# Optimization experiments

Measured on AMD Instinct MI355X. Metric: run time of the kernel, lower is better.

The kernel has to match this reference:

```python
import jax, jax.numpy as jnp
import numpy as np

N = 50000      # nodes
E = 800000     # edges (avg degree 16)
IN_DIM, HID, OUT = 128, 128, 64
EPS = 1e-5     # BatchNorm1d eps


def setup_inputs() -> dict:
    key = jax.random.key(0)
    ks = jax.random.split(key, 8)
    x = jax.random.normal(ks[0], (N, IN_DIM), jnp.float32)
    edge_index = jax.random.randint(ks[1], (2, E), 0, N, dtype=jnp.int32)
    def lin(k, i, o):
        return jax.random.normal(k, (i, o), jnp.float32) / np.sqrt(i).astype(np.float32)
    return {
        "x": x,
        "edge_index": edge_index,
        "W1": lin(ks[2], IN_DIM, HID), "b1": jnp.zeros((HID,), jnp.float32),
        "g1": jnp.ones((HID,), jnp.float32), "beta1": jnp.zeros((HID,), jnp.float32),
        "W2": lin(ks[3], HID, HID), "b2": jnp.zeros((HID,), jnp.float32),
        "g2": jnp.ones((HID,), jnp.float32), "beta2": jnp.zeros((HID,), jnp.float32),
        "W3": lin(ks[4], HID, OUT), "b3": jnp.zeros((OUT,), jnp.float32),
    }


def reference(x, edge_index, W1, b1, g1, beta1, W2, b2, g2, beta2, W3, b3):
    # GCNConv normalization: add self-loops, sym norm D^-1/2 (A+I) D^-1/2
    loops = jnp.arange(N, dtype=edge_index.dtype)
    src = jnp.concatenate([edge_index[0], loops])  # message sources
    dst = jnp.concatenate([edge_index[1], loops])  # aggregation targets
    deg = jax.ops.segment_sum(jnp.ones_like(dst, jnp.float32), dst, num_segments=N)
    dis = jnp.where(deg > 0, jax.lax.rsqrt(jnp.maximum(deg, 1.0)), 0.0)
    norm = dis[src] * dis[dst]  # [E+N]

    def conv(h, W, b):
        h = h @ W  # lin before propagation (PyG GCNConv)
        agg = jax.ops.segment_sum(h[src] * norm[:, None], dst, num_segments=N)
        return agg + b  # bias after aggregation

    def bn(h, g, beta):
        # training-mode BatchNorm1d: batch stats over node dim (biased var)
        m = h.mean(axis=0)
        v = h.var(axis=0)
        return g * (h - m) * jax.lax.rsqrt(v + EPS) + beta

    h = jax.nn.relu(bn(conv(x, W1, b1), g1, beta1))   # dropout deterministic (identity)
    h = jax.nn.relu(bn(conv(h, W2, b2), g2, beta2))
    h = conv(h, W3, b3)
    return jax.nn.log_softmax(h, axis=-1)
```

## Files before the change

### kernel.cpp

```cpp
#include <hip/hip_runtime.h>
#include <hip/hip_fp16.h>
#include <math.h>

#define N_NODES 50000
#define N_EDGES 800000
#define BN_EPS 1e-5f
#define CAP 64
#define NPART 256
#define PART 196
#define CHUNK_CAP 48

typedef _Float16 f16x8 __attribute__((ext_vector_type(8)));
typedef float f32x4 __attribute__((ext_vector_type(4)));

constexpr int GB = (N_NODES + 63) / 64;
constexpr int AB = (N_NODES + 3) / 4;
constexpr int EPB = N_EDGES / NPART;

__global__ __launch_bounds__(256) void setup_partA_k(
    const int* __restrict__ ei, unsigned int* __restrict__ chunk, int* __restrict__ cntT,
    const float* __restrict__ W1, const float* __restrict__ W2, const float* __restrict__ W3,
    __half* __restrict__ Wt1, __half* __restrict__ Wt2, __half* __restrict__ Wt3,
    int* __restrict__ fil, float* __restrict__ sums) {
    if (blockIdx.x < NPART) {
        __shared__ int cnt[NPART];
        int tid = threadIdx.x, b = blockIdx.x;
        cnt[tid] = 0;
        __syncthreads();
        int lo = b * EPB, hi = lo + EPB;
        for (int e = lo + tid; e < hi; e += 256) {
            int src = ei[e], dst = ei[N_EDGES + e];
            int p = dst / PART;
            int pos = atomicAdd(&cnt[p], 1);
            if (pos < CHUNK_CAP)
                chunk[(unsigned)((b << 8) + p) * CHUNK_CAP + pos] =
                    ((unsigned)dst << 16) | (unsigned)src;
        }
        __syncthreads();
        cntT[tid * NPART + b] = min(cnt[tid], CHUNK_CAP);
    } else {
        int i = (blockIdx.x - NPART) * 256 + threadIdx.x;
        if (i < N_NODES) fil[i] = 0;
        if (i < 512) sums[i] = 0.f;
        if (i < 16384) {
            int k = i >> 7, m = i & 127;
            Wt1[m * 128 + k] = __float2half(W1[i]);
            Wt2[m * 128 + k] = __float2half(W2[i]);
        }
        if (i < 8192) {
            int k = i >> 6, m = i & 63;
            Wt3[m * 128 + k] = __float2half(W3[i]);
        }
    }
}

template <int M, int AF32, int FUSE, int DSCALE>
__device__ __forceinline__ void gemm_body(int bid, int tid,
                                          const void* __restrict__ Av,
                                          const __half* __restrict__ Wt,
                                          const float* __restrict__ scale,
                                          const float* __restrict__ shift,
                                          const int* __restrict__ fil,
                                          __half* __restrict__ out) {
    constexpr int NF = M / 32;
    int wid = tid >> 6, lane = tid & 63;

    int rbase = bid * 64 + (wid >> 1) * 32;
    int ncol0 = (wid & 1) * (M / 2);
    int koff = (lane >> 4) * 8;

    int arow[2];
#pragma unroll
    for (int mi = 0; mi < 2; ++mi) {
        int r = rbase + mi * 16 + (lane & 15);
        arow[mi] = (r < N_NODES) ? r : (N_NODES - 1);
    }

    f32x4 acc[2][NF];
#pragma unroll
    for (int mi = 0; mi < 2; ++mi)
#pragma unroll
        for (int ni = 0; ni < NF; ++ni) acc[mi][ni] = (f32x4)(0.f);

#pragma unroll
    for (int k0 = 0; k0 < 128; k0 += 32) {
        float scv[8], shv[8];
        if constexpr (FUSE) {
            *(float4*)scv = *(const float4*)(scale + k0 + koff);
            *(float4*)(scv + 4) = *(const float4*)(scale + k0 + koff + 4);
            *(float4*)shv = *(const float4*)(shift + k0 + koff);
            *(float4*)(shv + 4) = *(const float4*)(shift + k0 + koff + 4);
        }
        f16x8 a[2], b[NF];
#pragma unroll
        for (int mi = 0; mi < 2; ++mi) {
            if constexpr (AF32) {
                const float* Af = (const float*)Av + (size_t)arow[mi] * 128 + k0 + koff;
                float4 p0 = *(const float4*)Af;
                float4 p1 = *(const float4*)(Af + 4);
                a[mi][0] = (_Float16)p0.x; a[mi][1] = (_Float16)p0.y;
                a[mi][2] = (_Float16)p0.z; a[mi][3] = (_Float16)p0.w;
                a[mi][4] = (_Float16)p1.x; a[mi][5] = (_Float16)p1.y;
                a[mi][6] = (_Float16)p1.z; a[mi][7] = (_Float16)p1.w;
            } else {
                f16x8 raw = *(const f16x8*)((const __half*)Av + (size_t)arow[mi] * 128 + k0 + koff);
                if constexpr (FUSE) {
#pragma unroll
                    for (int j = 0; j < 8; ++j)
                        a[mi][j] = (_Float16)fmaxf((float)raw[j] * scv[j] + shv[j], 0.f);
                } else {
                    a[mi] = raw;
                }
            }
        }
#pragma unroll
        for (int ni = 0; ni < NF; ++ni)
            b[ni] = *(const f16x8*)(Wt + (size_t)(ncol0 + ni * 16 + (lane & 15)) * 128 + k0 + koff);
#pragma unroll
        for (int mi = 0; mi < 2; ++mi)
#pragma unroll
            for (int ni = 0; ni < NF; ++ni)
                acc[mi][ni] = __builtin_amdgcn_mfma_f32_16x16x32_f16(a[mi], b[ni], acc[mi][ni], 0, 0, 0);
    }

    int ccol = ncol0 + (lane & 15);
#pragma unroll
    for (int mi = 0; mi < 2; ++mi)
#pragma unroll
        for (int q = 0; q < 4; ++q) {
            int grow = rbase + mi * 16 + (lane >> 4) * 4 + q;
            if (grow < N_NODES) {
                float ds = DSCALE ? rsqrtf((float)fil[grow] + 1.f) : 1.0f;
#pragma unroll
                for (int ni = 0; ni < NF; ++ni)
                    out[(size_t)grow * M + ccol + ni * 16] = __float2half(acc[mi][ni][q] * ds);
            }
        }
}

template <int M, int AF32, int FUSE, int DSCALE>
__global__ __launch_bounds__(256) void mfma_gemm_k(const void* __restrict__ Av,
                                                   const __half* __restrict__ Wt,
                                                   const float* __restrict__ scale,
                                                   const float* __restrict__ shift,
                                                   const int* __restrict__ fil,
                                                   __half* __restrict__ out) {
    gemm_body<M, AF32, FUSE, DSCALE>(blockIdx.x, threadIdx.x, Av, Wt, scale, shift, fil, out);
}

__global__ __launch_bounds__(256) void partB_gemm1_k(const float* __restrict__ x,
                                                     const __half* __restrict__ Wt1,
                                                     __half* __restrict__ outh,
                                                     const unsigned int* __restrict__ chunk,
                                                     const int* __restrict__ cntT,
                                                     int* __restrict__ fil,
                                                     unsigned short* __restrict__ bkt) {
    if (blockIdx.x < NPART) {
        int p = blockIdx.x, t = threadIdx.x;
        int n = cntT[p * NPART + t];
        const unsigned int* cp = chunk + (unsigned)((t << 8) + p) * CHUNK_CAP;
        for (int i = 0; i < n; ++i) {
            unsigned int u = cp[i];
            int dst = u >> 16, src = u & 0xffff;
            int pos = atomicAdd(&fil[dst], 1);
            if (pos < CAP) bkt[dst * CAP + pos] = (unsigned short)src;
        }
    } else {
        gemm_body<128, 1, 0, 0>(blockIdx.x - NPART, threadIdx.x, x, Wt1, nullptr, nullptr,
                                nullptr, outh);
    }
}

template <int SRCDIS>
__global__ __launch_bounds__(256) void aggh_k(const __half* __restrict__ hs,
                                              const int* __restrict__ fil,
                                              const unsigned short* __restrict__ bkt,
                                              const float* __restrict__ bias,
                                              __half* __restrict__ out) {
    int dst = blockIdx.x * 4 + (threadIdx.x >> 6);
    if (dst >= N_NODES) return;
    int lane = threadIdx.x & 63;
    int cnt = fil[dst];
    int n = min(cnt, CAP);
    float dd = rsqrtf((float)cnt + 1.f);
    const __half2* h2 = (const __half2*)hs;
    float2 v = __half22float2(h2[(size_t)dst * 64 + lane]);
    float ax, ay;
    if constexpr (SRCDIS) { ax = dd * v.x; ay = dd * v.y; }
    else { ax = v.x; ay = v.y; }
    const unsigned short* bp = bkt + (size_t)dst * CAP;
    int e = 0;
    for (; e + 4 <= n; e += 4) {
        int s0 = bp[e], s1 = bp[e + 1], s2 = bp[e + 2], s3 = bp[e + 3];
        float2 v0 = __half22float2(h2[(size_t)s0 * 64 + lane]);
        float2 v1 = __half22float2(h2[(size_t)s1 * 64 + lane]);
        float2 v2 = __half22float2(h2[(size_t)s2 * 64 + lane]);
        float2 v3 = __half22float2(h2[(size_t)s3 * 64 + lane]);
        if constexpr (SRCDIS) {
            float w0 = rsqrtf((float)fil[s0] + 1.f);
            float w1 = rsqrtf((float)fil[s1] + 1.f);
            float w2 = rsqrtf((float)fil[s2] + 1.f);
            float w3 = rsqrtf((float)fil[s3] + 1.f);
            ax += w0 * v0.x + w1 * v1.x + w2 * v2.x + w3 * v3.x;
            ay += w0 * v0.y + w1 * v1.y + w2 * v2.y + w3 * v3.y;
        } else {
            ax += (v0.x + v1.x) + (v2.x + v3.x);
            ay += (v0.y + v1.y) + (v2.y + v3.y);
        }
    }
    for (; e < n; ++e) {
        int s = bp[e];
        float2 vv = __half22float2(h2[(size_t)s * 64 + lane]);
        float w = SRCDIS ? rsqrtf((float)fil[s] + 1.f) : 1.0f;
        ax += w * vv.x;
        ay += w * vv.y;
    }
    float2 b = *(const float2*)(bias + lane * 2);
    ((__half2*)out)[(size_t)dst * 64 + lane] =
        __float22half2_rn(make_float2(dd * ax + b.x, dd * ay + b.y));
}

__global__ __launch_bounds__(256) void stats_k(const __half* __restrict__ h,
                                               float* __restrict__ sum, float* __restrict__ sq) {
    __shared__ float ssum[128], ssq[128];
    int tid = threadIdx.x;
    if (tid < 128) { ssum[tid] = 0.f; ssq[tid] = 0.f; }
    __syncthreads();
    float s[8], q[8];
#pragma unroll
    for (int j = 0; j < 8; ++j) { s[j] = 0.f; q[j] = 0.f; }
    const int total = N_NODES * 16;
    int stride = gridDim.x * blockDim.x;
    for (int i = blockIdx.x * blockDim.x + tid; i < total; i += stride) {
        f16x8 v = ((const f16x8*)h)[i];
#pragma unroll
        for (int j = 0; j < 8; ++j) {
            float f = (float)v[j];
            s[j] += f;
            q[j] += f * f;
        }
    }
#pragma unroll
    for (int j = 0; j < 8; ++j) {
        s[j] += __shfl_xor(s[j], 16); s[j] += __shfl_xor(s[j], 32);
        q[j] += __shfl_xor(q[j], 16); q[j] += __shfl_xor(q[j], 32);
    }
    int lane = tid & 63;
    if (lane < 16) {
        int c0 = lane * 8;
#pragma unroll
        for (int j = 0; j < 8; ++j) {
            atomicAdd(&ssum[c0 + j], s[j]);
            atomicAdd(&ssq[c0 + j], q[j]);
        }
    }
    __syncthreads();
    if (tid < 128) {
        atomicAdd(&sum[tid], ssum[tid]);
        atomicAdd(&sq[tid], ssq[tid]);
    }
}

__global__ void finalize_k(const float* __restrict__ sum, const float* __restrict__ sq,
                           const float* __restrict__ g, const float* __restrict__ beta,
                           float* scale, float* shift) {
    int f = threadIdx.x;
    float m = sum[f] * (1.0f / N_NODES);
    float v = sq[f] * (1.0f / N_NODES) - m * m;
    float sc = g[f] * rsqrtf(v + BN_EPS);
    scale[f] = sc;
    shift[f] = beta[f] - m * sc;
}

__global__ __launch_bounds__(256) void agg64sm_k(const __half* __restrict__ hs,
                                                 const int* __restrict__ fil,
                                                 const unsigned short* __restrict__ bkt,
                                                 const float* __restrict__ bias,
                                                 float* __restrict__ out) {
    int dst = blockIdx.x * 4 + (threadIdx.x >> 6);
    if (dst >= N_NODES) return;
    int lane = threadIdx.x & 63;
    int cnt = fil[dst];
    int n = min(cnt, CAP);
    float dd = rsqrtf((float)cnt + 1.f);
    float acc = __half2float(hs[(size_t)dst * 64 + lane]);
    const unsigned short* bp = bkt + (size_t)dst * CAP;
    int e = 0;
    for (; e + 4 <= n; e += 4) {
        int s0 = bp[e], s1 = bp[e + 1], s2 = bp[e + 2], s3 = bp[e + 3];
        float v0 = __half2float(hs[(size_t)s0 * 64 + lane]);
        float v1 = __half2float(hs[(size_t)s1 * 64 + lane]);
        float v2 = __half2float(hs[(size_t)s2 * 64 + lane]);
        float v3 = __half2float(hs[(size_t)s3 * 64 + lane]);
        acc += (v0 + v1) + (v2 + v3);
    }
    for (; e < n; ++e) acc += __half2float(hs[(size_t)bp[e] * 64 + lane]);
    float v = dd * acc + bias[lane];
    float m = v;
#pragma unroll
    for (int off = 32; off; off >>= 1) m = fmaxf(m, __shfl_xor(m, off));
    float p = expf(v - m);
    float ssum = p;
#pragma unroll
    for (int off = 32; off; off >>= 1) ssum += __shfl_xor(ssum, off);
    out[(size_t)dst * 64 + lane] = v - m - logf(ssum);
}

extern "C" void kernel_launch(void* const* d_in, const int* in_sizes, int n_in,
                              void* d_out, int out_size, void* d_ws, size_t ws_size,
                              hipStream_t stream) {
    const float* x = (const float*)d_in[0];
    const int* ei = (const int*)d_in[1];
    const float* W1 = (const float*)d_in[2];
    const float* b1 = (const float*)d_in[3];
    const float* g1 = (const float*)d_in[4];
    const float* be1 = (const float*)d_in[5];
    const float* W2 = (const float*)d_in[6];
    const float* b2 = (const float*)d_in[7];
    const float* g2 = (const float*)d_in[8];
    const float* be2 = (const float*)d_in[9];
    const float* W3 = (const float*)d_in[10];
    const float* b3 = (const float*)d_in[11];
    float* out = (float*)d_out;

    char* p = (char*)d_ws;
    auto alloc = [&](size_t bytes) {
        void* r = (void*)p;
        p += (bytes + 255) & ~(size_t)255;
        return r;
    };
    int* fil = (int*)alloc(N_NODES * 4);
    unsigned short* bkt = (unsigned short*)alloc((size_t)N_NODES * CAP * 2);
    unsigned int* chunk = (unsigned int*)alloc((size_t)NPART * NPART * CHUNK_CAP * 4);
    int* cntT = (int*)alloc(NPART * NPART * 4);
    float* sums = (float*)alloc(512 * 4);
    float* ss = (float*)alloc(512 * 4);
    __half* Wt1 = (__half*)alloc(128 * 128 * 2);
    __half* Wt2 = (__half*)alloc(128 * 128 * 2);
    __half* Wt3 = (__half*)alloc(64 * 128 * 2);
    __half* bufP = (__half*)alloc((size_t)N_NODES * 128 * 2);
    __half* bufQ = (__half*)alloc((size_t)N_NODES * 128 * 2);

    setup_partA_k<<<NPART + 196, 256, 0, stream>>>(ei, chunk, cntT, W1, W2, W3, Wt1, Wt2,
                                                   Wt3, fil, sums);

    partB_gemm1_k<<<NPART + GB, 256, 0, stream>>>(x, Wt1, bufQ, chunk, cntT, fil, bkt);
    aggh_k<1><<<AB, 256, 0, stream>>>(bufQ, fil, bkt, b1, bufP);
    stats_k<<<1024, 256, 0, stream>>>(bufP, sums, sums + 128);
    finalize_k<<<1, 128, 0, stream>>>(sums, sums + 128, g1, be1, ss, ss + 128);

    mfma_gemm_k<128, 0, 1, 1><<<GB, 256, 0, stream>>>(bufP, Wt2, ss, ss + 128, fil, bufQ);
    aggh_k<0><<<AB, 256, 0, stream>>>(bufQ, fil, bkt, b2, bufP);
    stats_k<<<1024, 256, 0, stream>>>(bufP, sums + 256, sums + 384);
    finalize_k<<<1, 128, 0, stream>>>(sums + 256, sums + 384, g2, be2, ss + 256, ss + 384);

    mfma_gemm_k<64, 0, 1, 1><<<GB, 256, 0, stream>>>(bufP, Wt3, ss + 256, ss + 384, fil, bufQ);
    agg64sm_k<<<AB, 256, 0, stream>>>(bufQ, fil, bkt, b3, out);
}
```

Baseline: 257.3 us.

## Vectorize gather aggregation with quarter-wave per neighbor and vectorized GEMM stores

The aggregation kernels now split each wave into four 16-lane groups, each gathering a different neighbor row with wide 16-byte (or 8-byte) loads, then combine the partial sums with cross-lane shuffles. The goal is fewer, wider memory transactions and more gathers in flight per wave than the old one-element-per-lane scheme. The GEMM swaps the MFMA operands so each lane holds four consecutive columns, which allows packed f16x4 stores instead of scalar half stores. The costs are extra shuffle reductions, idle lanes in the remainder handling, and only one quarter of the wave doing the final write.

```diff
diff --git a/kernel.cpp b/kernel.cpp
--- a/kernel.cpp
+++ b/kernel.cpp
@@ -11,6 +11,7 @@
 #define CHUNK_CAP 48
 
 typedef _Float16 f16x8 __attribute__((ext_vector_type(8)));
+typedef _Float16 f16x4 __attribute__((ext_vector_type(4)));
 typedef float f32x4 __attribute__((ext_vector_type(4)));
 
 constexpr int GB = (N_NODES + 63) / 64;
@@ -120,22 +121,24 @@
         for (int mi = 0; mi < 2; ++mi)
 #pragma unroll
             for (int ni = 0; ni < NF; ++ni)
-                acc[mi][ni] = __builtin_amdgcn_mfma_f32_16x16x32_f16(a[mi], b[ni], acc[mi][ni], 0, 0, 0);
-    }
-
-    int ccol = ncol0 + (lane & 15);
-#pragma unroll
-    for (int mi = 0; mi < 2; ++mi)
-#pragma unroll
-        for (int q = 0; q < 4; ++q) {
-            int grow = rbase + mi * 16 + (lane >> 4) * 4 + q;
-            if (grow < N_NODES) {
-                float ds = DSCALE ? rsqrtf((float)fil[grow] + 1.f) : 1.0f;
-#pragma unroll
-                for (int ni = 0; ni < NF; ++ni)
-                    out[(size_t)grow * M + ccol + ni * 16] = __float2half(acc[mi][ni][q] * ds);
+                acc[mi][ni] = __builtin_amdgcn_mfma_f32_16x16x32_f16(b[ni], a[mi], acc[mi][ni], 0, 0, 0);
+    }
+
+    int cg = lane >> 4;
+#pragma unroll
+    for (int mi = 0; mi < 2; ++mi) {
+        int grow = rbase + mi * 16 + (lane & 15);
+        if (grow < N_NODES) {
+            float ds = DSCALE ? rsqrtf((float)fil[grow] + 1.f) : 1.0f;
+#pragma unroll
+            for (int ni = 0; ni < NF; ++ni) {
+                f16x4 hv;
+#pragma unroll
+                for (int q = 0; q < 4; ++q) hv[q] = (_Float16)(acc[mi][ni][q] * ds);
+                *(f16x4*)(out + (size_t)grow * M + ncol0 + ni * 16 + cg * 4) = hv;
             }
         }
+    }
 }
 
 template <int M, int AF32, int FUSE, int DSCALE>
@@ -180,44 +183,74 @@
     int dst = blockIdx.x * 4 + (threadIdx.x >> 6);
     if (dst >= N_NODES) return;
     int lane = threadIdx.x & 63;
+    int qw = lane >> 4, li = lane & 15;
     int cnt = fil[dst];
     int n = min(cnt, CAP);
     float dd = rsqrtf((float)cnt + 1.f);
-    const __half2* h2 = (const __half2*)hs;
-    float2 v = __half22float2(h2[(size_t)dst * 64 + lane]);
-    float ax, ay;
-    if constexpr (SRCDIS) { ax = dd * v.x; ay = dd * v.y; }
-    else { ax = v.x; ay = v.y; }
+    const f16x8* h8 = (const f16x8*)hs;
+
+    float acc[8];
+    {
+        f16x8 sv = h8[(size_t)dst * 16 + li];
+        float selfw = (qw == 0) ? (SRCDIS ? dd : 1.f) : 0.f;
+#pragma unroll
+        for (int j = 0; j < 8; ++j) acc[j] = selfw * (float)sv[j];
+    }
+
     const unsigned short* bp = bkt + (size_t)dst * CAP;
     int e = 0;
+    for (; e + 8 <= n; e += 8) {
+        ushort4 ua = *(const ushort4*)(bp + e);
+        ushort4 ub = *(const ushort4*)(bp + e + 4);
+        int sa = (qw == 0) ? ua.x : (qw == 1) ? ua.y : (qw == 2) ? ua.z : ua.w;
+        int sb = (qw == 0) ? ub.x : (qw == 1) ? ub.y : (qw == 2) ? ub.z : ub.w;
+        f16x8 va = h8[(size_t)sa * 16 + li];
+        f16x8 vb = h8[(size_t)sb * 16 + li];
+        float wa = 1.f, wb = 1.f;
+        if constexpr (SRCDIS) {
+            wa = rsqrtf((float)fil[sa] + 1.f);
+            wb = rsqrtf((float)fil[sb] + 1.f);
+        }
+#pragma unroll
+        for (int j = 0; j < 8; ++j) acc[j] += wa * (float)va[j] + wb * (float)vb[j];
+    }
     for (; e + 4 <= n; e += 4) {
-        int s0 = bp[e], s1 = bp[e + 1], s2 = bp[e + 2], s3 = bp[e + 3];
-        float2 v0 = __half22float2(h2[(size_t)s0 * 64 + lane]);
-        float2 v1 = __half22float2(h2[(size_t)s1 * 64 + lane]);
-        float2 v2 = __half22float2(h2[(size_t)s2 * 64 + lane]);
-        float2 v3 = __half22float2(h2[(size_t)s3 * 64 + lane]);
-        if constexpr (SRCDIS) {
-            float w0 = rsqrtf((float)fil[s0] + 1.f);
-            float w1 = rsqrtf((float)fil[s1] + 1.f);
-            float w2 = rsqrtf((float)fil[s2] + 1.f);
-            float w3 = rsqrtf((float)fil[s3] + 1.f);
-            ax += w0 * v0.x + w1 * v1.x + w2 * v2.x + w3 * v3.x;
-            ay += w0 * v0.y + w1 * v1.y + w2 * v2.y + w3 * v3.y;
-        } else {
-            ax += (v0.x + v1.x) + (v2.x + v3.x);
-            ay += (v0.y + v1.y) + (v2.y + v3.y);
-        }
-    }
-    for (; e < n; ++e) {
-        int s = bp[e];
-        float2 vv = __half22float2(h2[(size_t)s * 64 + lane]);
-        float w = SRCDIS ? rsqrtf((float)fil[s] + 1.f) : 1.0f;
-        ax += w * vv.x;
-        ay += w * vv.y;
-    }
-    float2 b = *(const float2*)(bias + lane * 2);
-    ((__half2*)out)[(size_t)dst * 64 + lane] =
-        __float22half2_rn(make_float2(dd * ax + b.x, dd * ay + b.y));
+        ushort4 u = *(const ushort4*)(bp + e);
+        int s = (qw == 0) ? u.x : (qw == 1) ? u.y : (qw == 2) ? u.z : u.w;
+        f16x8 v = h8[(size_t)s * 16 + li];
+        float w = 1.f;
+        if constexpr (SRCDIS) w = rsqrtf((float)fil[s] + 1.f);
+#pragma unroll
+        for (int j = 0; j < 8; ++j) acc[j] += w * (float)v[j];
+    }
+    if (e < n) {
+        int rem = n - e;
+        ushort4 u = *(const ushort4*)(bp + e);
+        int s = (qw == 0) ? u.x : (qw == 1) ? u.y : (qw == 2) ? u.z : u.w;
+        if (qw < rem) {
+            f16x8 v = h8[(size_t)s * 16 + li];
+            float w = 1.f;
+            if constexpr (SRCDIS) w = rsqrtf((float)fil[s] + 1.f);
+#pragma unroll
+            for (int j = 0; j < 8; ++j) acc[j] += w * (float)v[j];
+        }
+    }
+
+#pragma unroll
+    for (int j = 0; j < 8; ++j) {
+        acc[j] += __shfl_xor(acc[j], 16);
+        acc[j] += __shfl_xor(acc[j], 32);
+    }
+
+    if (qw == 0) {
+        float bv[8];
+        *(float4*)bv = *(const float4*)(bias + li * 8);
+        *(float4*)(bv + 4) = *(const float4*)(bias + li * 8 + 4);
+        f16x8 o;
+#pragma unroll
+        for (int j = 0; j < 8; ++j) o[j] = (_Float16)(dd * acc[j] + bv[j]);
+        *(f16x8*)(out + (size_t)dst * 128 + li * 8) = o;
+    }
 }
 
 __global__ __launch_bounds__(256) void stats_k(const __half* __restrict__ h,
@@ -280,30 +313,74 @@
     int dst = blockIdx.x * 4 + (threadIdx.x >> 6);
     if (dst >= N_NODES) return;
     int lane = threadIdx.x & 63;
+    int qw = lane >> 4, li = lane & 15;
     int cnt = fil[dst];
     int n = min(cnt, CAP);
     float dd = rsqrtf((float)cnt + 1.f);
-    float acc = __half2float(hs[(size_t)dst * 64 + lane]);
+    const f16x4* h4 = (const f16x4*)hs;
+
+    float acc[4];
+    {
+        f16x4 sv = h4[(size_t)dst * 16 + li];
+        float selfw = (qw == 0) ? 1.f : 0.f;
+#pragma unroll
+        for (int j = 0; j < 4; ++j) acc[j] = selfw * (float)sv[j];
+    }
+
     const unsigned short* bp = bkt + (size_t)dst * CAP;
     int e = 0;
+    for (; e + 8 <= n; e += 8) {
+        ushort4 ua = *(const ushort4*)(bp + e);
+        ushort4 ub = *(const ushort4*)(bp + e + 4);
+        int sa = (qw == 0) ? ua.x : (qw == 1) ? ua.y : (qw == 2) ? ua.z : ua.w;
+        int sb = (qw == 0) ? ub.x : (qw == 1) ? ub.y : (qw == 2) ? ub.z : ub.w;
+        f16x4 va = h4[(size_t)sa * 16 + li];
+        f16x4 vb = h4[(size_t)sb * 16 + li];
+#pragma unroll
+        for (int j = 0; j < 4; ++j) acc[j] += (float)va[j] + (float)vb[j];
+    }
     for (; e + 4 <= n; e += 4) {
-        int s0 = bp[e], s1 = bp[e + 1], s2 = bp[e + 2], s3 = bp[e + 3];
-        float v0 = __half2float(hs[(size_t)s0 * 64 + lane]);
-        float v1 = __half2float(hs[(size_t)s1 * 64 + lane]);
-        float v2 = __half2float(hs[(size_t)s2 * 64 + lane]);
-        float v3 = __half2float(hs[(size_t)s3 * 64 + lane]);
-        acc += (v0 + v1) + (v2 + v3);
-    }
-    for (; e < n; ++e) acc += __half2float(hs[(size_t)bp[e] * 64 + lane]);
-    float v = dd * acc + bias[lane];
-    float m = v;
-#pragma unroll
-    for (int off = 32; off; off >>= 1) m = fmaxf(m, __shfl_xor(m, off));
-    float p = expf(v - m);
-    float ssum = p;
-#pragma unroll
-    for (int off = 32; off; off >>= 1) ssum += __shfl_xor(ssum, off);
-    out[(size_t)dst * 64 + lane] = v - m - logf(ssum);
+        ushort4 u = *(const ushort4*)(bp + e);
+        int s = (qw == 0) ? u.x : (qw == 1) ? u.y : (qw == 2) ? u.z : u.w;
+        f16x4 v = h4[(size_t)s * 16 + li];
+#pragma unroll
+        for (int j = 0; j < 4; ++j) acc[j] += (float)v[j];
+    }
+    if (e < n) {
+        int rem = n - e;
+        ushort4 u = *(const ushort4*)(bp + e);
+        int s = (qw == 0) ? u.x : (qw == 1) ? u.y : (qw == 2) ? u.z : u.w;
+        if (qw < rem) {
+            f16x4 v = h4[(size_t)s * 16 + li];
+#pragma unroll
+            for (int j = 0; j < 4; ++j) acc[j] += (float)v[j];
+        }
+    }
+
+#pragma unroll
+    for (int j = 0; j < 4; ++j) {
+        acc[j] += __shfl_xor(acc[j], 16);
+        acc[j] += __shfl_xor(acc[j], 32);
+    }
+
+    float bv[4];
+    *(float4*)bv = *(const float4*)(bias + li * 4);
+    float v[4];
+#pragma unroll
+    for (int j = 0; j < 4; ++j) v[j] = dd * acc[j] + bv[j];
+
+    float m = fmaxf(fmaxf(v[0], v[1]), fmaxf(v[2], v[3]));
+#pragma unroll
+    for (int off = 8; off; off >>= 1) m = fmaxf(m, __shfl_xor(m, off));
+    float p = expf(v[0] - m) + expf(v[1] - m) + expf(v[2] - m) + expf(v[3] - m);
+#pragma unroll
+    for (int off = 8; off; off >>= 1) p += __shfl_xor(p, off);
+    float lse = m + logf(p);
+
+    if (qw == 0) {
+        float4 o = make_float4(v[0] - lse, v[1] - lse, v[2] - lse, v[3] - lse);
+        *(float4*)(out + (size_t)dst * 64 + li * 4) = o;
+    }
 }
 
 extern "C" void kernel_launch(void* const* d_in, const int* in_sizes, int n_in,
```

New measurement: 253.4 us. No clear change (-1.5%).
